# Performance work log

Hardware: AMD Instinct MI355X
Metric: run time of the kernel (lower is better)

The kernel has to match this reference:

```python
import jax, jax.numpy as jnp
import numpy as np

V, C, L, D = 16384, 16, 6, 64  # n_vars, max_clauses, max_variables, embedding_dim


def _normalize(x):
    # utils.normalize: L2-normalize along the feature axis
    return x / jnp.linalg.norm(x, axis=-1, keepdims=True)


def _rescombine(x, W1, b1, W2, b2):
    # ResidualCombine: normalize(sigmoid(layer1(x)) + layer2(x))
    h = jax.nn.sigmoid(x @ W1 + b1) + x @ W2 + b2
    return _normalize(h)


def setup_inputs() -> dict:
    key = jax.random.key(0)
    ks = jax.random.split(key, 14)
    s = 0.05
    variables = jax.random.normal(ks[0], (V, D), jnp.float32)
    # literal variable indices; slot 0 of every clause is the owning variable i
    lits = jax.random.randint(ks[1], (V, C, L), 0, V)
    lits = lits.at[:, :, 0].set(jnp.arange(V)[:, None])
    neg_mask = jax.random.bernoulli(ks[2], 0.5, (V, C, L))
    # literal validity: at least 2 literals per clause, slot 0 always valid
    nvar = jax.random.randint(ks[3], (V, C), 2, L + 1)
    var_valid = jnp.arange(L)[None, None, :] < nvar[:, :, None]
    # clause validity: at least 1 clause per variable
    nclause = jax.random.randint(ks[4], (V,), 1, C + 1)
    clause_valid = jnp.arange(C)[None, :] < nclause[:, None]
    # params
    Wn = jax.random.normal(ks[5], (D, D), jnp.float32) * s
    bn = jnp.zeros((D,), jnp.float32)
    f = jax.random.normal(ks[6], (D,), jnp.float32)
    false_emb = f / jnp.linalg.norm(f)  # Embedding(1, D, max_norm=1.0)
    W1v = jax.random.normal(ks[7], (L * D, D), jnp.float32) * s
    b1v = jnp.zeros((D,), jnp.float32)
    W2v = jax.random.normal(ks[8], (L * D, D), jnp.float32) * s
    b2v = jnp.zeros((D,), jnp.float32)
    W1c = jax.random.normal(ks[9], (C * D, D), jnp.float32) * s
    b1c = jnp.zeros((D,), jnp.float32)
    W2c = jax.random.normal(ks[10], (C * D, D), jnp.float32) * s
    b2c = jnp.zeros((D,), jnp.float32)
    return dict(variables=variables, lits=lits, neg_mask=neg_mask, var_valid=var_valid,
                clause_valid=clause_valid, Wn=Wn, bn=bn, false_emb=false_emb,
                W1v=W1v, b1v=b1v, W2v=W2v, b2v=b2v, W1c=W1c, b1c=b1c, W2c=W2c, b2c=b2c)


def reference(variables, lits, neg_mask, var_valid, clause_valid,
              Wn, bn, false_emb, W1v, b1v, W2v, b2v, W1c, b1c, W2c, b2c):
    # gather literal embeddings: [V, C, L, D]
    g = variables[lits]
    # negation linear for negative literals
    v = jnp.where(neg_mask[..., None], g @ Wn + bn, g)
    # pad invalid literal slots with the 'false' embedding
    v = jnp.where(var_valid[..., None], v, false_emb)
    # variable_combiner over flattened [L*D]
    clause_emb = _rescombine(v.reshape(V, C, L * D), W1v, b1v, W2v, b2v)  # [V, C, D]
    # pad missing clauses with 'true' = negation(false)
    true_emb = false_emb @ Wn + bn
    clause_emb = jnp.where(clause_valid[..., None], clause_emb, true_emb)
    # clause_combiner over flattened [C*D]
    out = _rescombine(clause_emb.reshape(V, C * D), W1c, b1c, W2c, b2c)  # [V, D]
    # variables with no clauses pass through unchanged
    has_clauses = clause_valid.any(axis=-1)
    return jnp.where(has_clauses[:, None], out, variables)
```

## Files before the change

kernel.cpp:

```cpp
#include <hip/hip_runtime.h>
#include <hip/hip_bf16.h>

#define NV 16384
#define NC 16
#define NL 6
#define ND 64

typedef unsigned short u16;
typedef unsigned int u32;
typedef __attribute__((ext_vector_type(8))) short short8;
typedef __attribute__((ext_vector_type(4))) unsigned short u16x4;
typedef __attribute__((ext_vector_type(4))) float f32x4;

#define PB_BN  0
#define PB_FE  64
#define PB_B1V 128
#define PB_B2V 192
#define PB_B1C 256
#define PB_B2C 320
#define U_BVS   896
#define U_BCS   50048
#define U_BN    181120
#define U_VARSB 185216
#define U_NEGB  1233856
#define U_FIDX  2282496

__device__ __forceinline__ float ldbf(const u16* p, int i) {
  return __uint_as_float(((u32)p[i]) << 16);
}
__device__ __forceinline__ u16 f2b(float f) {
  u32 x = __float_as_uint(f);
  return (u16)((x + 0x7FFF + ((x >> 16) & 1)) >> 16);
}
__device__ __forceinline__ int ldmask(const void* p, int i, int bdt) {
  return bdt ? (int)((const signed char*)p)[i] : ((const int*)p)[i];
}
__device__ __forceinline__ int ldmask_nt(const void* p, int i, int bdt) {
  return bdt ? (int)__builtin_nontemporal_load((const signed char*)p + i)
             : __builtin_nontemporal_load((const int*)p + i);
}
__device__ __forceinline__ float ldf(const void* p, int i, int fdt) {
  return fdt ? ldbf((const u16*)p, i) : ((const float*)p)[i];
}
__device__ __forceinline__ void gll16(const u16* g, u16* l) {
  __builtin_amdgcn_global_load_lds(
      (const __attribute__((address_space(1))) u32*)(g),
      (__attribute__((address_space(3))) u32*)(l), 16, 0, 0);
}

__global__ __launch_bounds__(256) void k_prep(
    const void* vars, const int* __restrict__ lits, const void* negm, const void* vval,
    const void* Wn, const void* bn, const void* femb,
    const void* W1v, const void* b1v, const void* W2v, const void* b2v,
    const void* W1c, const void* b1c, const void* W2c, const void* b2c,
    int* flags, float* pbuf, u16* wsB) {
  __shared__ int s_cnt[4], s_big[4];
  const int t = threadIdx.x;
  {
    const u32 w = ((const u32*)vars)[t];
    const u32 e = (w >> 7) & 0xFF;
    const unsigned long long bal = __ballot(e >= 0x6E && e <= 0x8E);
    const u32 bw = ((const u32*)vval)[t];
    const unsigned long long bb = __ballot(bw > 1u);
    if ((t & 63) == 0) { s_cnt[t >> 6] = __popcll(bal); s_big[t >> 6] = (bb != 0ull); }
  }
  __syncthreads();
  const int fdt = (s_cnt[0] + s_cnt[1] + s_cnt[2] + s_cnt[3]) >= 192;
  const int bdt = (s_big[0] | s_big[1] | s_big[2] | s_big[3]);
  const int bid = blockIdx.x;

  if (bid == 0) {
    if (t == 0) { flags[0] = fdt; flags[1] = bdt; }
    if (t < 64) {
      const void* src[6] = {bn, femb, b1v, b2v, b1c, b2c};
      const int off[6] = {PB_BN, PB_FE, PB_B1V, PB_B2V, PB_B1C, PB_B2C};
      for (int j = 0; j < 6; j++) pbuf[off[j] + t] = ldf(src[j], t, fdt);
      wsB[U_VARSB + NV * 64 + t] = fdt ? ((const u16*)femb)[t] : f2b(((const float*)femb)[t]);
    }
  } else if (bid < 25) {
    const int c = (bid - 1) * 256 + t;
    const int ln = c & 63, nt = (c >> 6) & 7, ks = c >> 9;
    const int n = nt * 16 + (ln & 15);
    const void* src = (n < 64) ? W1v : W2v;
    const int kb = ks * 32 + (ln >> 4) * 8, n6 = n & 63;
    u16 o[8];
#pragma unroll
    for (int j = 0; j < 8; j++) o[j] = f2b(ldf(src, (kb + j) * 64 + n6, fdt));
    *(short8*)(wsB + U_BVS + c * 8) = *(short8*)o;
  } else if (bid < 89) {
    const int c = (bid - 25) * 256 + t;
    const int ln = c & 63, nt = (c >> 6) & 7, ks = c >> 9;
    const int n = nt * 16 + (ln & 15);
    const void* src = (n < 64) ? W1c : W2c;
    const int kb = ks * 32 + (ln >> 4) * 8, n6 = n & 63;
    u16 o[8];
#pragma unroll
    for (int j = 0; j < 8; j++) o[j] = f2b(ldf(src, (kb + j) * 64 + n6, fdt));
    *(short8*)(wsB + U_BCS + c * 8) = *(short8*)o;
  } else if (bid < 601) {
    const int c8 = (bid - 89) * 256 + t;
    u16 o[8];
    if (fdt) {
      *(short8*)o = ((const short8*)vars)[c8];
    } else {
      const float* f = (const float*)vars + c8 * 8;
#pragma unroll
      for (int j = 0; j < 8; j++) o[j] = f2b(f[j]);
    }
    *(short8*)(wsB + U_VARSB + c8 * 8) = *(short8*)o;
  } else if (bid < 2137) {
    const int i0 = ((bid - 601) * 256 + t) * 4;
    u16 o[4];
#pragma unroll
    for (int j = 0; j < 4; j++) {
      const int i = i0 + j;
      const int valid = ldmask(vval, i, bdt);
      const int neg = ldmask(negm, i, bdt);
      const int idx = lits[i];
      o[j] = (u16)(valid ? (idx + (neg ? (NV + 1) : 0)) : NV);
    }
    u16x4 ov = {o[0], o[1], o[2], o[3]};
    __builtin_nontemporal_store(ov, (u16x4*)(wsB + U_FIDX + i0));
  } else {
    const int nb = bid - 2137;
    const int lane = t & 63, wv = t >> 6;
    const int col = lane & 15, quad = lane >> 4, q8 = quad * 8;
    const int rowbase = nb * 64 + wv * 16;
    f32x4 acc[4];
#pragma unroll
    for (int nt = 0; nt < 4; nt++) acc[nt] = (f32x4){0.f, 0.f, 0.f, 0.f};
    const int arow = min(rowbase + col, NV);
#pragma unroll
    for (int ks = 0; ks < 2; ks++) {
      short8 a;
      if (arow == NV) {
#pragma unroll
        for (int j = 0; j < 8; j++) a[j] = (short)f2b(ldf(femb, ks * 32 + q8 + j, fdt));
      } else {
#pragma unroll
        for (int j = 0; j < 8; j++) a[j] = (short)f2b(ldf(vars, arow * 64 + ks * 32 + q8 + j, fdt));
      }
#pragma unroll
      for (int nt = 0; nt < 4; nt++) {
        short8 b;
#pragma unroll
        for (int j = 0; j < 8; j++)
          b[j] = (short)f2b(ldf(Wn, (ks * 32 + q8 + j) * 64 + nt * 16 + col, fdt));
        acc[nt] = __builtin_amdgcn_mfma_f32_16x16x32_bf16(a, b, acc[nt], 0, 0, 0);
      }
    }
#pragma unroll
    for (int reg = 0; reg < 4; reg++) {
      const int r = rowbase + quad * 4 + reg;
      if (r <= NV) {
#pragma unroll
        for (int nt = 0; nt < 4; nt++) {
          const int d = nt * 16 + col;
          wsB[U_NEGB + r * 64 + d] = f2b(acc[nt][reg] + ldf(bn, d, fdt));
        }
      }
    }
  }
}

__global__ __launch_bounds__(256, 2) void k_main(
    const void* __restrict__ vars, const void* __restrict__ cval,
    const float* __restrict__ pbuf, const int* __restrict__ flags,
    const u16* __restrict__ wsB, void* __restrict__ outv) {
  __shared__ __align__(16) u16 smem[24576];
  __shared__ float ps[16][4];
  __shared__ int hcS[16];

  const int tid = threadIdx.x, lane = tid & 63, wv = tid >> 6;
  const int col = lane & 15, quad = lane >> 4, q8 = quad * 8;
  const int fdt = flags[0], bdt = flags[1];
  const int vbase = (blockIdx.x * 4 + wv) * 4;
  const int v0 = blockIdx.x * 16;

  u32 r2_[4][3];
#pragma unroll
  for (int v4 = 0; v4 < 4; v4++)
#pragma unroll
    for (int i = 0; i < 3; i++)
      r2_[v4][i] = __builtin_nontemporal_load(
          (const u32*)(wsB + U_FIDX + (vbase + v4) * 96 + col * 6 + i * 2));

  const int cv = ldmask_nt(cval, vbase * 16 + lane, bdt);
  const unsigned long long bal = __ballot(cv != 0);
  if (lane < 4) hcS[wv * 4 + lane] = ((bal >> (lane * 16)) & 0xFFFFull) != 0;

  f32x4 acc[4][8];
#pragma unroll
  for (int v4 = 0; v4 < 4; v4++)
#pragma unroll
    for (int nt = 0; nt < 8; nt++) acc[v4][nt] = (f32x4){0.f, 0.f, 0.f, 0.f};

#pragma unroll
  for (int j = 0; j < 6; j++) {
    const int cl = wv * 6 + j;
    gll16(wsB + U_BVS + cl * 512 + lane * 8, &smem[cl * 512]);
  }
  short8 a_[3][4];
#pragma unroll
  for (int v4 = 0; v4 < 4; v4++) {
    const int idx = (int)(r2_[v4][0] & 0xFFFFu);
    a_[0][v4] = *(const short8*)(wsB + U_VARSB + idx * 64 + q8);
    a_[1][v4] = *(const short8*)(wsB + U_VARSB + idx * 64 + 32 + q8);
  }
  __syncthreads();

  for (int q = 0; q < 4; q++) {
    if (q < 3) {
#pragma unroll
      for (int j = 0; j < 6; j++) {
        const int cl = wv * 6 + j;
        gll16(wsB + U_BVS + (q + 1) * 12288 + cl * 512 + lane * 8,
              &smem[((q + 1) & 1) * 12288 + cl * 512]);
      }
    }
#pragma unroll
    for (int ksl = 0; ksl < 3; ksl++) {
      const int gk = q * 3 + ksl;
      const int gn = gk + 2;
      const int sf = (ksl + 2) % 3;
      if (gn < 12) {
        const int goff = (gn & 1) * 32 + q8;
        const int pi = gn >> 2, ph = (gn >> 1) & 1;
#pragma unroll
        for (int v4 = 0; v4 < 4; v4++) {
          const int idx = (int)((r2_[v4][pi] >> (ph * 16)) & 0xFFFFu);
          a_[sf][v4] = *(const short8*)(wsB + U_VARSB + idx * 64 + goff);
        }
      }
      __builtin_amdgcn_s_setprio(1);
#pragma unroll
      for (int nt = 0; nt < 8; nt++) {
        const short8 b = *(const short8*)(&smem[(q & 1) * 12288 + (ksl * 8 + nt) * 512 + lane * 8]);
#pragma unroll
        for (int v4 = 0; v4 < 4; v4++)
          acc[v4][nt] = __builtin_amdgcn_mfma_f32_16x16x32_bf16(a_[ksl][v4], b, acc[v4][nt], 0, 0, 0);
      }
      __builtin_amdgcn_s_setprio(0);
    }
    if (q < 3) __syncthreads();
  }
  __syncthreads();

  {
    float b1l[4], b2l[4], truel[4];
#pragma unroll
    for (int nt = 0; nt < 4; nt++) {
      const int d = nt * 16 + col;
      b1l[nt] = pbuf[PB_B1V + d];
      b2l[nt] = pbuf[PB_B2V + d];
      truel[nt] = ldbf(wsB, U_NEGB + NV * 64 + d);
    }
#pragma unroll
    for (int v4 = 0; v4 < 4; v4++) {
      const u32 vmask = (u32)((bal >> (v4 * 16)) & 0xFFFFull);
      const int vloc = wv * 4 + v4;
#pragma unroll
      for (int reg = 0; reg < 4; reg++) {
        const int c = quad * 4 + reg;
        float hh[4], ss = 0.f;
#pragma unroll
        for (int nt = 0; nt < 4; nt++) {
          hh[nt] = 1.0f / (1.0f + __expf(-(acc[v4][nt][reg] + b1l[nt]))) + acc[v4][nt + 4][reg] + b2l[nt];
          ss += hh[nt] * hh[nt];
        }
        ss += __shfl_xor(ss, 1, 64); ss += __shfl_xor(ss, 2, 64);
        ss += __shfl_xor(ss, 4, 64); ss += __shfl_xor(ss, 8, 64);
        const float sc = 1.0f / sqrtf(ss);
        const int valid = (vmask >> c) & 1;
#pragma unroll
        for (int nt = 0; nt < 4; nt++) {
          const float o = valid ? hh[nt] * sc : truel[nt];
          const int l2 = (nt * 2 + (col >> 3)) & 3;
          smem[(c * 2 + (nt >> 1)) * 512 + (l2 * 16 + vloc) * 8 + (col & 7)] = f2b(o);
        }
      }
    }
  }
  __syncthreads();

  f32x4 acc1 = (f32x4){0.f, 0.f, 0.f, 0.f}, acc2 = (f32x4){0.f, 0.f, 0.f, 0.f};
#pragma unroll 8
  for (int ks = 0; ks < 32; ks++) {
    const short8 a = *(const short8*)(&smem[ks * 512 + lane * 8]);
    const short8 b1 = *(const short8*)(wsB + U_BCS + (ks * 8 + wv) * 512 + lane * 8);
    const short8 b2 = *(const short8*)(wsB + U_BCS + (ks * 8 + wv + 4) * 512 + lane * 8);
    acc1 = __builtin_amdgcn_mfma_f32_16x16x32_bf16(a, b1, acc1, 0, 0, 0);
    acc2 = __builtin_amdgcn_mfma_f32_16x16x32_bf16(a, b2, acc2, 0, 0, 0);
  }

  const int d = wv * 16 + col;
  const float b1c_d = pbuf[PB_B1C + d], b2c_d = pbuf[PB_B2C + d];
  float h[4];
#pragma unroll
  for (int reg = 0; reg < 4; reg++) {
    h[reg] = 1.0f / (1.0f + __expf(-(acc1[reg] + b1c_d))) + acc2[reg] + b2c_d;
    float ssp = h[reg] * h[reg];
    ssp += __shfl_xor(ssp, 1, 64); ssp += __shfl_xor(ssp, 2, 64);
    ssp += __shfl_xor(ssp, 4, 64); ssp += __shfl_xor(ssp, 8, 64);
    if (col == 0) ps[quad * 4 + reg][wv] = ssp;
  }
  __syncthreads();
#pragma unroll
  for (int reg = 0; reg < 4; reg++) {
    const int r = quad * 4 + reg;
    const float tot = ps[r][0] + ps[r][1] + ps[r][2] + ps[r][3];
    float o = h[reg] * (1.0f / sqrtf(tot));
    const int oi = (v0 + r) * 64 + d;
    if (hcS[r]) {
      if (fdt) __builtin_nontemporal_store(f2b(o), &((u16*)outv)[oi]);
      else __builtin_nontemporal_store(o, &((float*)outv)[oi]);
    } else {
      if (fdt) __builtin_nontemporal_store(
          __builtin_nontemporal_load(&((const u16*)vars)[oi]), &((u16*)outv)[oi]);
      else __builtin_nontemporal_store(
          __builtin_nontemporal_load(&((const float*)vars)[oi]), &((float*)outv)[oi]);
    }
  }
}

extern "C" void kernel_launch(void* const* d_in, const int* in_sizes, int n_in,
                              void* d_out, int out_size, void* d_ws, size_t ws_size,
                              hipStream_t stream) {
  const void* vars = d_in[0];
  const int* lits = (const int*)d_in[1];
  const void* negm = d_in[2];
  const void* vval = d_in[3];
  const void* cvalid = d_in[4];
  const void* Wn = d_in[5];
  const void* bn = d_in[6];
  const void* femb = d_in[7];
  const void* W1v = d_in[8];
  const void* b1v = d_in[9];
  const void* W2v = d_in[10];
  const void* b2v = d_in[11];
  const void* W1c = d_in[12];
  const void* b1c = d_in[13];
  const void* W2c = d_in[14];
  const void* b2c = d_in[15];

  int* flags = (int*)d_ws;
  float* pbuf = (float*)((char*)d_ws + 256);
  u16* wsB = (u16*)d_ws;

  k_prep<<<2394, 256, 0, stream>>>(vars, lits, negm, vval, Wn, bn, femb,
                                   W1v, b1v, W2v, b2v, W1c, b1c, W2c, b2c,
                                   flags, pbuf, wsB);
  k_main<<<NV / 16, 256, 0, stream>>>(vars, cvalid, pbuf, flags, wsB, d_out);
}
```

Baseline: 158.0 us.

## Load first-stage weight fragments directly from global instead of LDS double-buffering

Drops the LDS double-buffered staging of the variable-combiner B weights and the block barriers it needed. Each wave now reads its B fragments straight from global memory (likely L2-resident, since all blocks share them) into registers every k-step. The shared-memory array shrinks, which could allow more resident blocks. In exchange, every wave re-fetches the weights from cache, adding global traffic and load latency inside the MFMA loop.

Result: slower. 163.2 us (+3.3%).

```diff
diff --git a/kernel.cpp b/kernel.cpp
--- a/kernel.cpp
+++ b/kernel.cpp
@@ -41,11 +41,6 @@
 }
 __device__ __forceinline__ float ldf(const void* p, int i, int fdt) {
   return fdt ? ldbf((const u16*)p, i) : ((const float*)p)[i];
-}
-__device__ __forceinline__ void gll16(const u16* g, u16* l) {
-  __builtin_amdgcn_global_load_lds(
-      (const __attribute__((address_space(1))) u32*)(g),
-      (__attribute__((address_space(3))) u32*)(l), 16, 0, 0);
 }
 
 __global__ __launch_bounds__(256) void k_prep(
@@ -167,7 +162,7 @@
     const void* __restrict__ vars, const void* __restrict__ cval,
     const float* __restrict__ pbuf, const int* __restrict__ flags,
     const u16* __restrict__ wsB, void* __restrict__ outv) {
-  __shared__ __align__(16) u16 smem[24576];
+  __shared__ __align__(16) u16 smem[16384];
   __shared__ float ps[16][4];
   __shared__ int hcS[16];
 
@@ -195,11 +190,6 @@
 #pragma unroll
     for (int nt = 0; nt < 8; nt++) acc[v4][nt] = (f32x4){0.f, 0.f, 0.f, 0.f};
 
-#pragma unroll
-  for (int j = 0; j < 6; j++) {
-    const int cl = wv * 6 + j;
-    gll16(wsB + U_BVS + cl * 512 + lane * 8, &smem[cl * 512]);
-  }
   short8 a_[3][4];
 #pragma unroll
   for (int v4 = 0; v4 < 4; v4++) {
@@ -207,44 +197,35 @@
     a_[0][v4] = *(const short8*)(wsB + U_VARSB + idx * 64 + q8);
     a_[1][v4] = *(const short8*)(wsB + U_VARSB + idx * 64 + 32 + q8);
   }
-  __syncthreads();
-
-  for (int q = 0; q < 4; q++) {
-    if (q < 3) {
-#pragma unroll
-      for (int j = 0; j < 6; j++) {
-        const int cl = wv * 6 + j;
-        gll16(wsB + U_BVS + (q + 1) * 12288 + cl * 512 + lane * 8,
-              &smem[((q + 1) & 1) * 12288 + cl * 512]);
-      }
-    }
-#pragma unroll
-    for (int ksl = 0; ksl < 3; ksl++) {
-      const int gk = q * 3 + ksl;
-      const int gn = gk + 2;
-      const int sf = (ksl + 2) % 3;
-      if (gn < 12) {
-        const int goff = (gn & 1) * 32 + q8;
-        const int pi = gn >> 2, ph = (gn >> 1) & 1;
-#pragma unroll
-        for (int v4 = 0; v4 < 4; v4++) {
-          const int idx = (int)((r2_[v4][pi] >> (ph * 16)) & 0xFFFFu);
-          a_[sf][v4] = *(const short8*)(wsB + U_VARSB + idx * 64 + goff);
-        }
-      }
-      __builtin_amdgcn_s_setprio(1);
-#pragma unroll
-      for (int nt = 0; nt < 8; nt++) {
-        const short8 b = *(const short8*)(&smem[(q & 1) * 12288 + (ksl * 8 + nt) * 512 + lane * 8]);
-#pragma unroll
-        for (int v4 = 0; v4 < 4; v4++)
-          acc[v4][nt] = __builtin_amdgcn_mfma_f32_16x16x32_bf16(a_[ksl][v4], b, acc[v4][nt], 0, 0, 0);
-      }
-      __builtin_amdgcn_s_setprio(0);
-    }
-    if (q < 3) __syncthreads();
-  }
-  __syncthreads();
+
+  const u16* __restrict__ Bg = wsB + U_BVS;
+#pragma unroll
+  for (int gk = 0; gk < 12; gk++) {
+    const int su = gk % 3;
+    const int sf = (gk + 2) % 3;
+    const int gn = gk + 2;
+    if (gn < 12) {
+      const int goff = (gn & 1) * 32 + q8;
+      const int pi = gn >> 2, ph = (gn >> 1) & 1;
+#pragma unroll
+      for (int v4 = 0; v4 < 4; v4++) {
+        const int idx = (int)((r2_[v4][pi] >> (ph * 16)) & 0xFFFFu);
+        a_[sf][v4] = *(const short8*)(wsB + U_VARSB + idx * 64 + goff);
+      }
+    }
+    short8 bl[8];
+#pragma unroll
+    for (int nt = 0; nt < 8; nt++)
+      bl[nt] = *(const short8*)(Bg + (gk * 8 + nt) * 512 + lane * 8);
+    __builtin_amdgcn_s_setprio(1);
+#pragma unroll
+    for (int nt = 0; nt < 8; nt++) {
+#pragma unroll
+      for (int v4 = 0; v4 < 4; v4++)
+        acc[v4][nt] = __builtin_amdgcn_mfma_f32_16x16x32_bf16(a_[su][v4], bl[nt], acc[v4][nt], 0, 0, 0);
+    }
+    __builtin_amdgcn_s_setprio(0);
+  }
 
   {
     float b1l[4], b2l[4], truel[4];
```
